# Kernel tuning notes

Hardware: AMD Instinct MI355X
Metric: run time of the kernel (lower is better)

The kernel has to match this reference:

```python
import jax, jax.numpy as jnp
import numpy as np

U, E, V = 1024, 256, 20200

def _w(key, shape):
    fan_in = shape[0] if len(shape) > 1 else shape[0]
    return jax.random.normal(key, shape, dtype=jnp.float32) * (1.0 / np.sqrt(fan_in))

def setup_inputs() -> dict:
    key = jax.random.key(0)
    ks = jax.random.split(key, 20)
    inp = {
        'enc_in': jax.random.randint(ks[0], (32, 64), 0, V),
        'teacher': jax.random.randint(ks[1], (32, 16), 0, V),
        'max_cmd_len': 16,
        'batch_size': 32,
        # encoder params
        'Ee': jax.random.normal(ks[2], (V, E), dtype=jnp.float32) * 0.02,
        'enc_Wx': _w(ks[3], (E, 3 * U)),
        'enc_Wh': _w(ks[4], (U, 3 * U)),
        'enc_b_in': jnp.zeros((3 * U,), jnp.float32),
        'enc_b_rec': jnp.zeros((3 * U,), jnp.float32),
        # decoder params
        'Ed': jax.random.normal(ks[5], (V, E), dtype=jnp.float32) * 0.02,
        'dec_Wx': _w(ks[6], (U + E, 3 * U)),
        'dec_Wh': _w(ks[7], (U, 3 * U)),
        'dec_b_in': jnp.zeros((3 * U,), jnp.float32),
        'dec_b_rec': jnp.zeros((3 * U,), jnp.float32),
        # Bahdanau attention params
        'W1': _w(ks[8], (U, U)), 'b1': jnp.zeros((U,), jnp.float32),
        'W2': _w(ks[9], (U, U)), 'b2': jnp.zeros((U,), jnp.float32),
        'Va': _w(ks[10], (U, 1)), 'bv': jnp.zeros((1,), jnp.float32),
        # output projection
        'Wf': _w(ks[11], (U, V)), 'bf': jnp.zeros((V,), jnp.float32),
    }
    return inp

def gru_step(x, h, Wx, Wh, b_in, b_rec):
    # Keras GRU, reset_after=True, gate order (z, r, h)
    gx = x @ Wx + b_in          # [B, 3U]
    gh = h @ Wh + b_rec         # [B, 3U]
    xz, xr, xh = jnp.split(gx, 3, axis=-1)
    hz, hr, hh = jnp.split(gh, 3, axis=-1)
    z = jax.nn.sigmoid(xz + hz)
    r = jax.nn.sigmoid(xr + hr)
    c = jnp.tanh(xh + r * hh)
    return z * h + (1.0 - z) * c

def reference(enc_in, teacher, max_cmd_len, batch_size,
              Ee, enc_Wx, enc_Wh, enc_b_in, enc_b_rec,
              Ed, dec_Wx, dec_Wh, dec_b_in, dec_b_rec,
              W1, b1, W2, b2, Va, bv, Wf, bf):
    B = enc_in.shape[0]
    # ----- encoder: GRU over source, h0 = 0 -----
    x_emb = Ee[enc_in]                          # [B, S, E]
    def enc_step(h, x_t):
        h_new = gru_step(x_t, h, enc_Wx, enc_Wh, enc_b_in, enc_b_rec)
        return h_new, h_new
    enc_hidden, enc_seq = jax.lax.scan(enc_step, jnp.zeros((B, U), x_emb.dtype),
                                       jnp.swapaxes(x_emb, 0, 1))
    encoded = jnp.swapaxes(enc_seq, 0, 1)       # [B, S, U]

    # ----- decoder: teacher-forced, attention each step -----
    pre_enc = encoded @ W1 + b1                 # precompute W1(encoded): [B, S, U]
    h0_dec = jnp.zeros((B, U), encoded.dtype)   # original calls gru without initial_state

    def dec_step(dec_h, tok):
        q = dec_h @ W2 + b2                                     # [B, U]
        score = jnp.tanh(pre_enc + q[:, None, :]) @ Va + bv     # [B, S, 1]
        attn = jax.nn.softmax(score, axis=1)
        ctx = jnp.sum(attn * encoded, axis=1)                   # [B, U]
        x = jnp.concatenate([ctx, Ed[tok]], axis=-1)            # [B, U+E]
        h_new = gru_step(x, h0_dec, dec_Wx, dec_Wh, dec_b_in, dec_b_rec)
        logits_t = h_new @ Wf + bf                              # [B, V]
        return h_new, logits_t

    toks = jnp.swapaxes(teacher[:, :max_cmd_len], 0, 1)         # [T, B]
    _, logits_tbv = jax.lax.scan(dec_step, enc_hidden, toks)    # [T, B, V]
    logits = jnp.swapaxes(logits_tbv, 0, 1)                     # [B, T, V]
    predictions = jnp.argmax(logits, axis=-1).astype(jnp.int64) # [B, T]
    return logits, predictions
```

## Files before the change

kernel.cpp:

```cpp
#include <hip/hip_runtime.h>
#include <cmath>

#define BB 32
#define SS 64
#define TT 16
#define UU 1024
#define EE 256
#define VV 20200
#define G3 3072
#define NBLK 256

#define WS_XEMBT 0
#define WS_HT    (WS_XEMBT + SS*EE*BB)
#define WS_ENC   (WS_HT + 2*UU*BB)
#define WS_PRE   (WS_ENC + BB*SS*UU)
#define WS_Q     (WS_PRE + BB*SS*UU)
#define WS_ESC   (WS_Q + BB*UU)
#define WS_XT    (WS_ESC + BB*SS)
#define WS_HDT   (WS_XT + UU*BB)
#define WS_HD    (WS_HDT + UU*BB)
#define WS_DEMB  (WS_HD + BB*TT*UU)
#define WS_GXD   (WS_DEMB + BB*TT*EE)
#define WS_BAR   (WS_GXD + BB*TT*G3)

#define ACC4(A, V, S) do { (A).x += (V).x * (S); (A).y += (V).y * (S); \
                           (A).z += (V).z * (S); (A).w += (V).w * (S); } while (0)
#define RED4(A, M) do { (A).x += __shfl_xor((A).x, M, 64); (A).y += __shfl_xor((A).y, M, 64); \
                        (A).z += __shfl_xor((A).z, M, 64); (A).w += __shfl_xor((A).w, M, 64); } while (0)

__device__ __forceinline__ float sigmoidf_(float x) {
    return 1.0f / (1.0f + expf(-x));
}

__device__ __forceinline__ void store_agent(float* p, float v) {
    __hip_atomic_store(p, v, __ATOMIC_RELAXED, __HIP_MEMORY_SCOPE_AGENT);
}

__device__ __forceinline__ void grid_barrier(unsigned* base, int grp, unsigned g) {
    __syncthreads();
    if (threadIdx.x == 0) {
        const unsigned p = g & 1u;
        unsigned* cnt  = base + ((unsigned)grp * 2u + p) * 32u;
        unsigned* root = base + (16u + p) * 32u;
        unsigned* gen  = base + (18u + (unsigned)grp) * 32u;
        __builtin_amdgcn_s_waitcnt(0);
        bool done = false;
        unsigned a = __hip_atomic_fetch_add(cnt, 1u, __ATOMIC_RELAXED, __HIP_MEMORY_SCOPE_AGENT);
        if (a == 31u) {
            __hip_atomic_store(cnt, 0u, __ATOMIC_RELAXED, __HIP_MEMORY_SCOPE_AGENT);
            unsigned r = __hip_atomic_fetch_add(root, 1u, __ATOMIC_RELAXED, __HIP_MEMORY_SCOPE_AGENT);
            if (r == 7u) {
                __hip_atomic_store(root, 0u, __ATOMIC_RELAXED, __HIP_MEMORY_SCOPE_AGENT);
                #pragma unroll
                for (unsigned gg = 0; gg < 8; ++gg)
                    __hip_atomic_store(base + (18u + gg) * 32u, g + 1u,
                                       __ATOMIC_RELAXED, __HIP_MEMORY_SCOPE_AGENT);
                done = true;
            }
        }
        if (!done) {
            while (__hip_atomic_load(gen, __ATOMIC_RELAXED, __HIP_MEMORY_SCOPE_AGENT) <= g) {
                __builtin_amdgcn_s_sleep(4);
            }
        }
        __builtin_amdgcn_fence(__ATOMIC_ACQUIRE, "agent");
    }
    __syncthreads();
}

__global__ __launch_bounds__(256) void k_prep(const int* __restrict__ enc_in,
                                              const float* __restrict__ Ee,
                                              const int* __restrict__ teacher,
                                              const float* __restrict__ Ed,
                                              float* __restrict__ ws) {
    int gid = blockIdx.x * 256 + threadIdx.x;
    const int NE = SS * EE * BB;
    const int NH = UU * BB;
    const int ND = BB * TT * EE;
    if (gid < NE) {
        int b = gid & 31;
        int e = (gid >> 5) & 255;
        int s = gid >> 13;
        ws[WS_XEMBT + gid] = Ee[(size_t)enc_in[b * SS + s] * EE + e];
    } else if (gid < NE + NH) {
        ws[WS_HT + (gid - NE)] = 0.0f;
    } else if (gid < NE + NH + ND) {
        int idx = gid - NE - NH;
        int e = idx & 255;
        int row = idx >> 8;
        int t = row >> 5, b = row & 31;
        ws[WS_DEMB + idx] = Ed[(size_t)teacher[b * TT + t] * EE + e];
    } else if (gid < NE + NH + ND + 3072) {
        ((unsigned*)(ws + WS_BAR))[gid - NE - NH - ND] = 0u;
    }
}

__global__ __launch_bounds__(512, 2) void k_encoder(const float* __restrict__ Wh,
                                                    const float* __restrict__ Wx,
                                                    const float* __restrict__ b_in,
                                                    const float* __restrict__ b_rec,
                                                    float* __restrict__ ws) {
    float* XembT = ws + WS_XEMBT;
    float* hT = ws + WS_HT;
    float* enc = ws + WS_ENC;
    unsigned* bar = (unsigned*)(ws + WS_BAR);

    __shared__ float Whs[12288];
    __shared__ float Wxs[3072];
    __shared__ float scr[4096];

    const int tid = threadIdx.x;
    const int bid = blockIdx.x;
    const int grp = bid & 7;
    const int wv = tid >> 6;
    const int lane = tid & 63;
    const int kp = lane & 7;
    const int rg = lane >> 3;

    for (int k = tid; k < 1024; k += 512) {
        #pragma unroll
        for (int g = 0; g < 3; ++g)
            *(float4*)(Whs + k * 12 + g * 4) =
                *(const float4*)(Wh + (size_t)k * G3 + g * 1024 + bid * 4);
    }
    if (tid < 256) {
        int k = tid;
        #pragma unroll
        for (int g = 0; g < 3; ++g)
            *(float4*)(Wxs + k * 12 + g * 4) =
                *(const float4*)(Wx + (size_t)k * G3 + g * 1024 + bid * 4);
    }

    float bz_s = 0.f, br_s = 0.f, bci_s = 0.f, bcr_s = 0.f;
    int rc_ = 0, rb_ = 0, rj_ = 0;
    if (tid < 128) {
        rc_ = tid >> 5; rb_ = tid & 31; rj_ = bid * 4 + rc_;
        bz_s = b_in[rj_] + b_rec[rj_];
        br_s = b_in[1024 + rj_] + b_rec[1024 + rj_];
        bci_s = b_in[2048 + rj_];
        bcr_s = b_rec[2048 + rj_];
    }
    __syncthreads();

    const int hk0 = wv * 128 + kp;
    const int xk0 = wv * 32 + kp;

    for (int t = 0; t < SS; ++t) {
        const float* hprev = hT + (t & 1) * (UU * BB);
        float* hnext = hT + ((t & 1) ^ 1) * (UU * BB);

        float4 az[4], ar[4], ah[4], ax[4];
        #pragma unroll
        for (int c = 0; c < 4; ++c) {
            az[c] = make_float4(0.f, 0.f, 0.f, 0.f);
            ar[c] = make_float4(0.f, 0.f, 0.f, 0.f);
            ah[c] = make_float4(0.f, 0.f, 0.f, 0.f);
            ax[c] = make_float4(0.f, 0.f, 0.f, 0.f);
        }

        {
            const float* hp = hprev + hk0 * 32 + rg * 4;
            float4 hb[16];
            #pragma unroll
            for (int u = 0; u < 16; ++u) hb[u] = *(const float4*)(hp + u * 256);
            #pragma unroll
            for (int u = 0; u < 16; ++u) {
                const float* wp = Whs + (hk0 + 8 * u) * 12;
                float4 wz = *(const float4*)wp;
                float4 wr_ = *(const float4*)(wp + 4);
                float4 wc_ = *(const float4*)(wp + 8);
                float4 hv = hb[u];
                ACC4(az[0], hv, wz.x); ACC4(az[1], hv, wz.y); ACC4(az[2], hv, wz.z); ACC4(az[3], hv, wz.w);
                ACC4(ar[0], hv, wr_.x); ACC4(ar[1], hv, wr_.y); ACC4(ar[2], hv, wr_.z); ACC4(ar[3], hv, wr_.w);
                ACC4(ah[0], hv, wc_.x); ACC4(ah[1], hv, wc_.y); ACC4(ah[2], hv, wc_.z); ACC4(ah[3], hv, wc_.w);
            }
        }
        {
            const float* xp = XembT + t * (EE * BB) + xk0 * 32 + rg * 4;
            float4 xb[4];
            #pragma unroll
            for (int u = 0; u < 4; ++u) xb[u] = *(const float4*)(xp + u * 256);
            #pragma unroll
            for (int u = 0; u < 4; ++u) {
                const float* wp = Wxs + (xk0 + 8 * u) * 12;
                float4 wz = *(const float4*)wp;
                float4 wr_ = *(const float4*)(wp + 4);
                float4 wc_ = *(const float4*)(wp + 8);
                float4 xv = xb[u];
                ACC4(az[0], xv, wz.x); ACC4(az[1], xv, wz.y); ACC4(az[2], xv, wz.z); ACC4(az[3], xv, wz.w);
                ACC4(ar[0], xv, wr_.x); ACC4(ar[1], xv, wr_.y); ACC4(ar[2], xv, wr_.z); ACC4(ar[3], xv, wr_.w);
                ACC4(ax[0], xv, wc_.x); ACC4(ax[1], xv, wc_.y); ACC4(ax[2], xv, wc_.z); ACC4(ax[3], xv, wc_.w);
            }
        }
        #pragma unroll
        for (int m = 1; m <= 4; m <<= 1) {
            #pragma unroll
            for (int c = 0; c < 4; ++c) { RED4(az[c], m); RED4(ar[c], m); RED4(ah[c], m); RED4(ax[c], m); }
        }
        if (kp == 0) {
            float* sb = scr + wv * 512 + rg * 4;
            #pragma unroll
            for (int c = 0; c < 4; ++c) {
                *(float4*)(sb + c * 32) = az[c];
                *(float4*)(sb + 128 + c * 32) = ar[c];
                *(float4*)(sb + 256 + c * 32) = ah[c];
                *(float4*)(sb + 384 + c * 32) = ax[c];
            }
        }
        __syncthreads();
        if (tid < 128) {
            float saz = 0.f, sar = 0.f, sah = 0.f, sax = 0.f;
            #pragma unroll
            for (int w = 0; w < 8; ++w) {
                const float* sb = scr + w * 512 + rc_ * 32 + rb_;
                saz += sb[0]; sar += sb[128]; sah += sb[256]; sax += sb[384];
            }
            float z = sigmoidf_(saz + bz_s);
            float r = sigmoidf_(sar + br_s);
            float cc = tanhf(sax + bci_s + r * (sah + bcr_s));
            float hold = hprev[rj_ * 32 + rb_];
            float hnew = z * hold + (1.0f - z) * cc;
            store_agent(&hnext[rj_ * 32 + rb_], hnew);
            enc[((size_t)rb_ * SS + t) * UU + rj_] = hnew;
        }
        grid_barrier(bar, grp, (unsigned)t);
    }
}

__global__ __launch_bounds__(256) void k_gemm(const float* __restrict__ A,
                                              const float* __restrict__ Bm,
                                              const float* __restrict__ bias,
                                              float* __restrict__ C,
                                              int M, int N, int K) {
    __shared__ float As[16][68];
    __shared__ float Bs[16][132];
    const int rb = blockIdx.x * 64;
    const int cb = blockIdx.y * 128;
    const int tid = threadIdx.x;
    const int cg = tid & 31;
    const int rg = tid >> 5;
    float acc[8][4] = {{0.f}};

    const int arow = tid >> 2, akq = (tid & 3) * 4;
    const int bkk = tid >> 4, bc8 = (tid & 15) * 8;
    const bool nfull = (cb + 128 <= N);

    for (int k0 = 0; k0 < K; k0 += 16) {
        {
            float4 a4 = *(const float4*)(A + (size_t)(rb + arow) * K + k0 + akq);
            As[akq + 0][arow] = a4.x; As[akq + 1][arow] = a4.y;
            As[akq + 2][arow] = a4.z; As[akq + 3][arow] = a4.w;
        }
        {
            int col = cb + bc8;
            const float* bp = Bm + (size_t)(k0 + bkk) * N + col;
            if (nfull) {
                float4 x0 = *(const float4*)bp;
                float4 x1 = *(const float4*)(bp + 4);
                Bs[bkk][bc8 + 0] = x0.x; Bs[bkk][bc8 + 1] = x0.y; Bs[bkk][bc8 + 2] = x0.z; Bs[bkk][bc8 + 3] = x0.w;
                Bs[bkk][bc8 + 4] = x1.x; Bs[bkk][bc8 + 5] = x1.y; Bs[bkk][bc8 + 6] = x1.z; Bs[bkk][bc8 + 7] = x1.w;
            } else {
                #pragma unroll
                for (int jj = 0; jj < 8; ++jj)
                    Bs[bkk][bc8 + jj] = (col + jj < N) ? bp[jj] : 0.0f;
            }
        }
        __syncthreads();
        #pragma unroll
        for (int kk = 0; kk < 16; ++kk) {
            float4 a0 = *(const float4*)&As[kk][rg * 8];
            float4 a1 = *(const float4*)&As[kk][rg * 8 + 4];
            float4 b0 = *(const float4*)&Bs[kk][cg * 4];
            float av[8] = {a0.x, a0.y, a0.z, a0.w, a1.x, a1.y, a1.z, a1.w};
            float bv[4] = {b0.x, b0.y, b0.z, b0.w};
            #pragma unroll
            for (int i = 0; i < 8; ++i)
                #pragma unroll
                for (int jj = 0; jj < 4; ++jj)
                    acc[i][jj] += av[i] * bv[jj];
        }
        __syncthreads();
    }
    const int col0 = cb + cg * 4;
    const bool cfull = (col0 + 4 <= N);
    #pragma unroll
    for (int i = 0; i < 8; ++i) {
        int row = rb + rg * 8 + i;
        float* cp = C + (size_t)row * N + col0;
        if (cfull) {
            float4 o;
            o.x = acc[i][0] + bias[col0 + 0];
            o.y = acc[i][1] + bias[col0 + 1];
            o.z = acc[i][2] + bias[col0 + 2];
            o.w = acc[i][3] + bias[col0 + 3];
            *(float4*)cp = o;
        } else {
            #pragma unroll
            for (int jj = 0; jj < 4; ++jj)
                if (col0 + jj < N) cp[jj] = acc[i][jj] + bias[col0 + jj];
        }
    }
}

__global__ __launch_bounds__(256, 1) void k_decoder(const float* __restrict__ W2,
                                                    const float* __restrict__ b2,
                                                    const float* __restrict__ Va,
                                                    const float* __restrict__ bv,
                                                    const float* __restrict__ Wxd,
                                                    const float* __restrict__ b_rec,
                                                    float* __restrict__ ws) {
    float* hT = ws + WS_HT;
    float* enc = ws + WS_ENC;
    float* pre = ws + WS_PRE;
    float* q = ws + WS_Q;
    float* esc = ws + WS_ESC;
    float* xT = ws + WS_XT;
    float* hdT = ws + WS_HDT;
    float* Hd = ws + WS_HD;
    float* GXd = ws + WS_GXD;
    unsigned* bar = (unsigned*)(ws + WS_BAR) + 1024;

    __shared__ float Wxds[12288];
    __shared__ float W2s[4096];
    __shared__ float scr[1536];
    __shared__ float eL[64];
    __shared__ float attnL[64];
    __shared__ float shs[256];

    const int tid = threadIdx.x;
    const int bid = blockIdx.x;
    const int grp = bid & 7;
    const int wv = tid >> 6;
    const int lane = tid & 63;
    const int kp = lane & 7;
    const int rg = lane >> 3;

    for (int k = tid; k < 1024; k += 256) {
        #pragma unroll
        for (int g = 0; g < 3; ++g)
            *(float4*)(Wxds + k * 12 + g * 4) =
                *(const float4*)(Wxd + (size_t)k * G3 + g * 1024 + bid * 4);
        *(float4*)(W2s + k * 4) = *(const float4*)(W2 + (size_t)k * UU + bid * 4);
    }

    float bzr_s = 0.f, brr_s = 0.f, bcr_s = 0.f;
    int rc_ = 0, rb_ = 0, rj_ = 0;
    if (tid < 128) {
        rc_ = tid >> 5; rb_ = tid & 31; rj_ = bid * 4 + rc_;
        bzr_s = b_rec[rj_];
        brr_s = b_rec[1024 + rj_];
        bcr_s = b_rec[2048 + rj_];
    }
    __syncthreads();

    const int xk0 = wv * 256 + kp;
    unsigned bc = 0;

    for (int t = 0; t < TT; ++t) {
        const float* hsrc = (t == 0) ? hT : hdT;

        {
            const int cq = lane & 3;
            const int kpq = (lane >> 2) & 7;
            const int rgq = (lane >> 5) | (wv << 1);
            const int qc = bid * 4 + cq;
            const float* hp = hsrc + kpq * 32 + rgq * 4;
            float a0 = 0, a1 = 0, a2 = 0, a3 = 0;
            for (int g = 0; g < 16; ++g) {
                float4 hv[8]; float wr[8];
                #pragma unroll
                for (int u = 0; u < 8; ++u) {
                    hv[u] = *(const float4*)(hp + (g * 8 + u) * 256);
                    wr[u] = W2s[(kpq + 8 * (g * 8 + u)) * 4 + cq];
                }
                #pragma unroll
                for (int u = 0; u < 8; ++u) {
                    a0 += hv[u].x * wr[u]; a1 += hv[u].y * wr[u];
                    a2 += hv[u].z * wr[u]; a3 += hv[u].w * wr[u];
                }
            }
            #pragma unroll
            for (int m = 4; m <= 16; m <<= 1) {
                a0 += __shfl_xor(a0, m, 64); a1 += __shfl_xor(a1, m, 64);
                a2 += __shfl_xor(a2, m, 64); a3 += __shfl_xor(a3, m, 64);
            }
            if (kpq == 0) {
                float bb2 = b2[qc];
                store_agent(&q[(size_t)(rgq * 4 + 0) * UU + qc], a0 + bb2);
                store_agent(&q[(size_t)(rgq * 4 + 1) * UU + qc], a1 + bb2);
                store_agent(&q[(size_t)(rgq * 4 + 2) * UU + qc], a2 + bb2);
                store_agent(&q[(size_t)(rgq * 4 + 3) * UU + qc], a3 + bb2);
            }
        }
        grid_barrier(bar, grp, bc++);

        {
            const int b = bid >> 3, s0 = (bid & 7) * 8;
            const int pi = tid >> 5, kq = tid & 31;
            const int srow = s0 + pi;
            const float* pe = pre + ((size_t)b * SS + srow) * UU;
            const float* qb = q + (size_t)b * UU;
            float acc = 0;
            #pragma unroll
            for (int kk = 0; kk < 8; ++kk) {
                int k = kq * 32 + kk * 4;
                float4 p4 = *(const float4*)(pe + k);
                float4 q4 = *(const float4*)(qb + k);
                float4 v4 = *(const float4*)(Va + k);
                acc += tanhf(p4.x + q4.x) * v4.x + tanhf(p4.y + q4.y) * v4.y +
                       tanhf(p4.z + q4.z) * v4.z + tanhf(p4.w + q4.w) * v4.w;
            }
            #pragma unroll
            for (int m = 16; m >= 1; m >>= 1) acc += __shfl_xor(acc, m, 32);
            if (kq == 0) store_agent(&esc[b * SS + srow], acc + bv[0]);
        }
        grid_barrier(bar, grp, bc++);

        {
            const int b = bid >> 3, ug = bid & 7;
            if (tid < 64) eL[tid] = esc[b * SS + tid];
            __syncthreads();
            if (tid < 64) {
                float v = eL[tid];
                float m = v;
                #pragma unroll
                for (int mm = 32; mm >= 1; mm >>= 1) m = fmaxf(m, __shfl_xor(m, mm, 64));
                float p = expf(v - m);
                float sum = p;
                #pragma unroll
                for (int mm = 32; mm >= 1; mm >>= 1) sum += __shfl_xor(sum, mm, 64);
                attnL[tid] = p / sum;
            }
            __syncthreads();
            const int u = ug * 128 + (tid & 127), sp = tid >> 7;
            float acc = 0;
            #pragma unroll 8
            for (int i = 0; i < 32; ++i) {
                int srow = sp * 32 + i;
                acc += attnL[srow] * enc[((size_t)b * SS + srow) * UU + u];
            }
            shs[(tid & 127) * 2 + sp] = acc;
            __syncthreads();
            if (tid < 128)
                store_agent(&xT[(size_t)(ug * 128 + tid) * BB + b], shs[tid * 2] + shs[tid * 2 + 1]);
        }
        grid_barrier(bar, grp, bc++);

        {
            float4 sz[4], sr_[4], sc_[4];
            #pragma unroll
            for (int c = 0; c < 4; ++c) {
                sz[c] = make_float4(0.f, 0.f, 0.f, 0.f);
                sr_[c] = make_float4(0.f, 0.f, 0.f, 0.f);
                sc_[c] = make_float4(0.f, 0.f, 0.f, 0.f);
            }
            const float* xp = xT + xk0 * 32 + rg * 4;
            #pragma unroll
            for (int gg = 0; gg < 2; ++gg) {
                float4 xb[16];
                #pragma unroll
                for (int u = 0; u < 16; ++u) xb[u] = *(const float4*)(xp + (gg * 16 + u) * 256);
                #pragma unroll
                for (int u = 0; u < 16; ++u) {
                    const float* wp = Wxds + (xk0 + 8 * (gg * 16 + u)) * 12;
                    float4 wz = *(const float4*)wp;
                    float4 wr4 = *(const float4*)(wp + 4);
                    float4 wc4 = *(const float4*)(wp + 8);
                    float4 xv = xb[u];
                    ACC4(sz[0], xv, wz.x); ACC4(sz[1], xv, wz.y); ACC4(sz[2], xv, wz.z); ACC4(sz[3], xv, wz.w);
                    ACC4(sr_[0], xv, wr4.x); ACC4(sr_[1], xv, wr4.y); ACC4(sr_[2], xv, wr4.z); ACC4(sr_[3], xv, wr4.w);
                    ACC4(sc_[0], xv, wc4.x); ACC4(sc_[1], xv, wc4.y); ACC4(sc_[2], xv, wc4.z); ACC4(sc_[3], xv, wc4.w);
                }
            }
            #pragma unroll
            for (int m = 1; m <= 4; m <<= 1) {
                #pragma unroll
                for (int c = 0; c < 4; ++c) { RED4(sz[c], m); RED4(sr_[c], m); RED4(sc_[c], m); }
            }
            if (kp == 0) {
                float* sb = scr + wv * 384 + rg * 4;
                #pragma unroll
                for (int c = 0; c < 4; ++c) {
                    *(float4*)(sb + c * 32) = sz[c];
                    *(float4*)(sb + 128 + c * 32) = sr_[c];
                    *(float4*)(sb + 256 + c * 32) = sc_[c];
                }
            }
            __syncthreads();
            if (tid < 128) {
                float ssz = 0.f, ssr = 0.f, ssc = 0.f;
                #pragma unroll
                for (int w = 0; w < 4; ++w) {
                    const float* sb = scr + w * 384 + rc_ * 32 + rb_;
                    ssz += sb[0]; ssr += sb[128]; ssc += sb[256];
                }
                const float* gx = GXd + (size_t)(t * BB + rb_) * G3;
                float z = sigmoidf_(ssz + gx[rj_] + bzr_s);
                float rr = sigmoidf_(ssr + gx[1024 + rj_] + brr_s);
                float cc = tanhf(ssc + gx[2048 + rj_] + rr * bcr_s);
                float h = (1.0f - z) * cc;
                Hd[((size_t)rb_ * TT + t) * UU + rj_] = h;
                store_agent(&hdT[(size_t)rj_ * BB + rb_], h);
            }
        }
        grid_barrier(bar, grp, bc++);
    }
}

__global__ __launch_bounds__(256) void k_argmax(const float* __restrict__ logits,
                                                float* __restrict__ outp) {
    const int row = blockIdx.x;
    const float* lr = logits + (size_t)row * VV;
    const int tid = threadIdx.x;
    float best = -INFINITY;
    int bidx = 0x7fffffff;
    for (int c = tid; c < VV; c += 256) {
        float v = lr[c];
        if (v > best) { best = v; bidx = c; }
    }
    __shared__ float bv_[256];
    __shared__ int bi_[256];
    bv_[tid] = best; bi_[tid] = bidx;
    __syncthreads();
    for (int s2 = 128; s2 > 0; s2 >>= 1) {
        if (tid < s2) {
            float ov = bv_[tid + s2]; int oi = bi_[tid + s2];
            if (ov > bv_[tid] || (ov == bv_[tid] && oi < bi_[tid])) {
                bv_[tid] = ov; bi_[tid] = oi;
            }
        }
        __syncthreads();
    }
    if (tid == 0) outp[row] = (float)bi_[0];
}

extern "C" void kernel_launch(void* const* d_in, const int* in_sizes, int n_in,
                              void* d_out, int out_size, void* d_ws, size_t ws_size,
                              hipStream_t stream) {
    const int* enc_in = (const int*)d_in[0];
    const int* teacher = (const int*)d_in[1];
    const float* Ee = (const float*)d_in[4];
    const float* eWx = (const float*)d_in[5];
    const float* eWh = (const float*)d_in[6];
    const float* eb_in = (const float*)d_in[7];
    const float* eb_rec = (const float*)d_in[8];
    const float* Ed = (const float*)d_in[9];
    const float* dWx = (const float*)d_in[10];
    const float* db_in = (const float*)d_in[12];
    const float* db_rec = (const float*)d_in[13];
    const float* W1 = (const float*)d_in[14];
    const float* b1 = (const float*)d_in[15];
    const float* W2 = (const float*)d_in[16];
    const float* b2 = (const float*)d_in[17];
    const float* Va = (const float*)d_in[18];
    const float* bvv = (const float*)d_in[19];
    const float* Wf = (const float*)d_in[20];
    const float* bf = (const float*)d_in[21];
    float* ws = (float*)d_ws;
    float* out = (float*)d_out;

    const int NTOT = SS * EE * BB + UU * BB + BB * TT * EE + 3072;
    k_prep<<<dim3((NTOT + 255) / 256), dim3(256), 0, stream>>>(enc_in, Ee, teacher, Ed, ws);

    k_gemm<<<dim3(8, 24), dim3(256), 0, stream>>>(ws + WS_DEMB, dWx + (size_t)UU * G3, db_in,
                                                  ws + WS_GXD, BB * TT, G3, EE);

    k_encoder<<<dim3(NBLK), dim3(512), 0, stream>>>(eWh, eWx, eb_in, eb_rec, ws);

    k_gemm<<<dim3(32, 8), dim3(256), 0, stream>>>(ws + WS_ENC, W1, b1, ws + WS_PRE, BB * SS, UU, UU);

    k_decoder<<<dim3(NBLK), dim3(256), 0, stream>>>(W2, b2, Va, bvv, dWx, db_rec, ws);

    k_gemm<<<dim3(8, 158), dim3(256), 0, stream>>>(ws + WS_HD, Wf, bf, out, BB * TT, VV, UU);

    k_argmax<<<dim3(BB * TT), dim3(256), 0, stream>>>(out, out + (size_t)BB * TT * VV);
}
```

Before: 2.044 ms.

## Replace atomic-counter grid barrier with flag-based hierarchical barrier, add 128x128 output GEMM

Replaces the fetch-add counter grid barrier with a per-block flag barrier: each block writes its generation, group leaders poll 32 flags with a wavefront vote, and block 0 aggregates and releases the groups. The encoder keeps the previous hidden value in a register instead of reloading it from global memory. The decoder prefetches its input-gate values before the attention phases, and the final vocab projection uses a new 128x128-tile GEMM. A stray `wz.x * 0.f` term is added to one accumulation, which is harmless but odd. The barrier layout reuses the existing workspace barrier region, whose size must fit the new flag indices.

```diff
diff --git a/kernel.cpp b/kernel.cpp
--- a/kernel.cpp
+++ b/kernel.cpp
@@ -35,32 +35,42 @@
 __device__ __forceinline__ void store_agent(float* p, float v) {
     __hip_atomic_store(p, v, __ATOMIC_RELAXED, __HIP_MEMORY_SCOPE_AGENT);
 }
-
-__device__ __forceinline__ void grid_barrier(unsigned* base, int grp, unsigned g) {
+__device__ __forceinline__ void store_agent_u(unsigned* p, unsigned v) {
+    __hip_atomic_store(p, v, __ATOMIC_RELAXED, __HIP_MEMORY_SCOPE_AGENT);
+}
+__device__ __forceinline__ unsigned load_agent_u(unsigned* p) {
+    return __hip_atomic_load(p, __ATOMIC_RELAXED, __HIP_MEMORY_SCOPE_AGENT);
+}
+
+__device__ __forceinline__ void grid_barrier(unsigned* base, int bid, unsigned g) {
     __syncthreads();
-    if (threadIdx.x == 0) {
-        const unsigned p = g & 1u;
-        unsigned* cnt  = base + ((unsigned)grp * 2u + p) * 32u;
-        unsigned* root = base + (16u + p) * 32u;
-        unsigned* gen  = base + (18u + (unsigned)grp) * 32u;
-        __builtin_amdgcn_s_waitcnt(0);
-        bool done = false;
-        unsigned a = __hip_atomic_fetch_add(cnt, 1u, __ATOMIC_RELAXED, __HIP_MEMORY_SCOPE_AGENT);
-        if (a == 31u) {
-            __hip_atomic_store(cnt, 0u, __ATOMIC_RELAXED, __HIP_MEMORY_SCOPE_AGENT);
-            unsigned r = __hip_atomic_fetch_add(root, 1u, __ATOMIC_RELAXED, __HIP_MEMORY_SCOPE_AGENT);
-            if (r == 7u) {
-                __hip_atomic_store(root, 0u, __ATOMIC_RELAXED, __HIP_MEMORY_SCOPE_AGENT);
-                #pragma unroll
-                for (unsigned gg = 0; gg < 8; ++gg)
-                    __hip_atomic_store(base + (18u + gg) * 32u, g + 1u,
-                                       __ATOMIC_RELAXED, __HIP_MEMORY_SCOPE_AGENT);
-                done = true;
-            }
-        }
-        if (!done) {
-            while (__hip_atomic_load(gen, __ATOMIC_RELAXED, __HIP_MEMORY_SCOPE_AGENT) <= g) {
-                __builtin_amdgcn_s_sleep(4);
+    if (threadIdx.x < 64) {
+        const int lane = threadIdx.x;
+        const int grp = bid >> 5;
+        const unsigned gv = g + 1u;
+        if (lane == 0) {
+            __builtin_amdgcn_s_waitcnt(0);
+            store_agent_u(base + bid, gv);
+        }
+        if ((bid & 31) == 0) {
+            for (;;) {
+                unsigned v = load_agent_u(base + grp * 32 + (lane & 31));
+                if (__all((int)(v >= gv))) break;
+                __builtin_amdgcn_s_sleep(2);
+            }
+            if (lane == 0) store_agent_u(base + 256 + grp * 32, gv);
+            if (bid == 0) {
+                for (;;) {
+                    unsigned v = load_agent_u(base + 256 + (lane & 7) * 32);
+                    if (__all((int)(v >= gv))) break;
+                    __builtin_amdgcn_s_sleep(2);
+                }
+                if (lane < 8) store_agent_u(base + 512 + lane * 32, gv);
+            }
+        }
+        if (bid != 0) {
+            while (load_agent_u(base + 512 + grp * 32) < gv) {
+                __builtin_amdgcn_s_sleep(2);
             }
         }
         __builtin_amdgcn_fence(__ATOMIC_ACQUIRE, "agent");
@@ -111,7 +121,6 @@
 
     const int tid = threadIdx.x;
     const int bid = blockIdx.x;
-    const int grp = bid & 7;
     const int wv = tid >> 6;
     const int lane = tid & 63;
     const int kp = lane & 7;
@@ -144,6 +153,7 @@
 
     const int hk0 = wv * 128 + kp;
     const int xk0 = wv * 32 + kp;
+    float hreg = 0.f;
 
     for (int t = 0; t < SS; ++t) {
         const float* hprev = hT + (t & 1) * (UU * BB);
@@ -189,7 +199,7 @@
                 float4 xv = xb[u];
                 ACC4(az[0], xv, wz.x); ACC4(az[1], xv, wz.y); ACC4(az[2], xv, wz.z); ACC4(az[3], xv, wz.w);
                 ACC4(ar[0], xv, wr_.x); ACC4(ar[1], xv, wr_.y); ACC4(ar[2], xv, wr_.z); ACC4(ar[3], xv, wr_.w);
-                ACC4(ax[0], xv, wc_.x); ACC4(ax[1], xv, wc_.y); ACC4(ax[2], xv, wc_.z); ACC4(ax[3], xv, wc_.w);
+                ACC4(ax[0], xv, wz.x * 0.f + wc_.x); ACC4(ax[1], xv, wc_.y); ACC4(ax[2], xv, wc_.z); ACC4(ax[3], xv, wc_.w);
             }
         }
         #pragma unroll
@@ -218,12 +228,12 @@
             float z = sigmoidf_(saz + bz_s);
             float r = sigmoidf_(sar + br_s);
             float cc = tanhf(sax + bci_s + r * (sah + bcr_s));
-            float hold = hprev[rj_ * 32 + rb_];
-            float hnew = z * hold + (1.0f - z) * cc;
+            float hnew = z * hreg + (1.0f - z) * cc;
+            hreg = hnew;
             store_agent(&hnext[rj_ * 32 + rb_], hnew);
             enc[((size_t)rb_ * SS + t) * UU + rj_] = hnew;
         }
-        grid_barrier(bar, grp, (unsigned)t);
+        grid_barrier(bar, bid, (unsigned)t);
     }
 }
 
@@ -297,6 +307,89 @@
         } else {
             #pragma unroll
             for (int jj = 0; jj < 4; ++jj)
+                if (col0 + jj < N) cp[jj] = acc[i][jj] + bias[col0 + jj];
+        }
+    }
+}
+
+__global__ __launch_bounds__(256) void k_gemm128(const float* __restrict__ A,
+                                                 const float* __restrict__ Bm,
+                                                 const float* __restrict__ bias,
+                                                 float* __restrict__ C,
+                                                 int M, int N, int K) {
+    __shared__ float As[16][132];
+    __shared__ float Bs[16][132];
+    const int rb = blockIdx.x * 128;
+    const int cb = blockIdx.y * 128;
+    const int tid = threadIdx.x;
+    const int rg = tid >> 4;
+    const int cg = tid & 15;
+    float acc[8][8] = {{0.f}};
+
+    const int arow = tid >> 1, akq = (tid & 1) * 8;
+    const int bkk = tid >> 4, bc8 = (tid & 15) * 8;
+    const bool nfull = (cb + 128 <= N);
+
+    for (int k0 = 0; k0 < K; k0 += 16) {
+        {
+            const float* ap = A + (size_t)(rb + arow) * K + k0 + akq;
+            float4 a0 = *(const float4*)ap;
+            float4 a1 = *(const float4*)(ap + 4);
+            As[akq + 0][arow] = a0.x; As[akq + 1][arow] = a0.y;
+            As[akq + 2][arow] = a0.z; As[akq + 3][arow] = a0.w;
+            As[akq + 4][arow] = a1.x; As[akq + 5][arow] = a1.y;
+            As[akq + 6][arow] = a1.z; As[akq + 7][arow] = a1.w;
+        }
+        {
+            int col = cb + bc8;
+            const float* bp = Bm + (size_t)(k0 + bkk) * N + col;
+            if (nfull) {
+                *(float4*)&Bs[bkk][bc8] = *(const float4*)bp;
+                *(float4*)&Bs[bkk][bc8 + 4] = *(const float4*)(bp + 4);
+            } else {
+                #pragma unroll
+                for (int jj = 0; jj < 8; ++jj)
+                    Bs[bkk][bc8 + jj] = (col + jj < N) ? bp[jj] : 0.0f;
+            }
+        }
+        __syncthreads();
+        #pragma unroll
+        for (int kk = 0; kk < 16; ++kk) {
+            float4 a0 = *(const float4*)&As[kk][rg * 8];
+            float4 a1 = *(const float4*)&As[kk][rg * 8 + 4];
+            float4 b0 = *(const float4*)&Bs[kk][cg * 8];
+            float4 b1 = *(const float4*)&Bs[kk][cg * 8 + 4];
+            float av[8] = {a0.x, a0.y, a0.z, a0.w, a1.x, a1.y, a1.z, a1.w};
+            float bw[8] = {b0.x, b0.y, b0.z, b0.w, b1.x, b1.y, b1.z, b1.w};
+            #pragma unroll
+            for (int i = 0; i < 8; ++i)
+                #pragma unroll
+                for (int jj = 0; jj < 8; ++jj)
+                    acc[i][jj] += av[i] * bw[jj];
+        }
+        __syncthreads();
+    }
+    const int col0 = cb + cg * 8;
+    const bool cfull = (col0 + 8 <= N);
+    #pragma unroll
+    for (int i = 0; i < 8; ++i) {
+        int row = rb + rg * 8 + i;
+        float* cp = C + (size_t)row * N + col0;
+        if (cfull) {
+            float4 o0, o1;
+            o0.x = acc[i][0] + bias[col0 + 0];
+            o0.y = acc[i][1] + bias[col0 + 1];
+            o0.z = acc[i][2] + bias[col0 + 2];
+            o0.w = acc[i][3] + bias[col0 + 3];
+            o1.x = acc[i][4] + bias[col0 + 4];
+            o1.y = acc[i][5] + bias[col0 + 5];
+            o1.z = acc[i][6] + bias[col0 + 6];
+            o1.w = acc[i][7] + bias[col0 + 7];
+            *(float4*)cp = o0;
+            *(float4*)(cp + 4) = o1;
+        } else {
+            #pragma unroll
+            for (int jj = 0; jj < 8; ++jj)
                 if (col0 + jj < N) cp[jj] = acc[i][jj] + bias[col0 + jj];
         }
     }
@@ -329,7 +422,6 @@
 
     const int tid = threadIdx.x;
     const int bid = blockIdx.x;
-    const int grp = bid & 7;
     const int wv = tid >> 6;
     const int lane = tid & 63;
     const int kp = lane & 7;
@@ -358,6 +450,14 @@
 
     for (int t = 0; t < TT; ++t) {
         const float* hsrc = (t == 0) ? hT : hdT;
+
+        float gxz = 0.f, gxr = 0.f, gxc = 0.f;
+        if (tid < 128) {
+            const float* gx = GXd + (size_t)(t * BB + rb_) * G3;
+            gxz = gx[rj_];
+            gxr = gx[1024 + rj_];
+            gxc = gx[2048 + rj_];
+        }
 
         {
             const int cq = lane & 3;
@@ -392,7 +492,7 @@
                 store_agent(&q[(size_t)(rgq * 4 + 3) * UU + qc], a3 + bb2);
             }
         }
-        grid_barrier(bar, grp, bc++);
+        grid_barrier(bar, bid, bc++);
 
         {
             const int b = bid >> 3, s0 = (bid & 7) * 8;
@@ -414,7 +514,7 @@
             for (int m = 16; m >= 1; m >>= 1) acc += __shfl_xor(acc, m, 32);
             if (kq == 0) store_agent(&esc[b * SS + srow], acc + bv[0]);
         }
-        grid_barrier(bar, grp, bc++);
+        grid_barrier(bar, bid, bc++);
 
         {
             const int b = bid >> 3, ug = bid & 7;
@@ -444,7 +544,7 @@
             if (tid < 128)
                 store_agent(&xT[(size_t)(ug * 128 + tid) * BB + b], shs[tid * 2] + shs[tid * 2 + 1]);
         }
-        grid_barrier(bar, grp, bc++);
+        grid_barrier(bar, bid, bc++);
 
         {
             float4 sz[4], sr_[4], sc_[4];
@@ -494,16 +594,15 @@
                     const float* sb = scr + w * 384 + rc_ * 32 + rb_;
                     ssz += sb[0]; ssr += sb[128]; ssc += sb[256];
                 }
-                const float* gx = GXd + (size_t)(t * BB + rb_) * G3;
-                float z = sigmoidf_(ssz + gx[rj_] + bzr_s);
-                float rr = sigmoidf_(ssr + gx[1024 + rj_] + brr_s);
-                float cc = tanhf(ssc + gx[2048 + rj_] + rr * bcr_s);
+                float z = sigmoidf_(ssz + gxz + bzr_s);
+                float rr = sigmoidf_(ssr + gxr + brr_s);
+                float cc = tanhf(ssc + gxc + rr * bcr_s);
                 float h = (1.0f - z) * cc;
                 Hd[((size_t)rb_ * TT + t) * UU + rj_] = h;
                 store_agent(&hdT[(size_t)rj_ * BB + rb_], h);
             }
         }
-        grid_barrier(bar, grp, bc++);
+        grid_barrier(bar, bid, bc++);
     }
 }
 
@@ -571,7 +670,7 @@
 
     k_decoder<<<dim3(NBLK), dim3(256), 0, stream>>>(W2, b2, Va, bvv, dWx, db_rec, ws);
 
-    k_gemm<<<dim3(8, 158), dim3(256), 0, stream>>>(ws + WS_HD, Wf, bf, out, BB * TT, VV, UU);
+    k_gemm128<<<dim3(4, 158), dim3(256), 0, stream>>>(ws + WS_HD, Wf, bf, out, BB * TT, VV, UU);
 
     k_argmax<<<dim3(BB * TT), dim3(256), 0, stream>>>(out, out + (size_t)BB * TT * VV);
 }
```

Result: slower. 2.098 ms (+2.6%).
